# Kernel optimization log

Measured on AMD Instinct MI355X. Metric: run time of the kernel, lower is better.

The kernel has to match this reference:

```python
import jax, jax.numpy as jnp
import numpy as np
import math

N_NODES = 50000
N_EDGES = 640000
IN_FEATS = 128
HEADS = 8
OUT_FEATS = 16
D_FF = 4 * IN_FEATS


def setup_inputs() -> dict:
    key = jax.random.key(0)
    ks = jax.random.split(key, 10)
    s = 0.05
    return {
        "feat": jax.random.normal(ks[0], (N_NODES, IN_FEATS), jnp.float32),
        "src": jax.random.randint(ks[1], (N_EDGES,), 0, N_NODES, jnp.int32),
        "dst": jax.random.randint(ks[2], (N_EDGES,), 0, N_NODES, jnp.int32),
        "Wq": jax.random.normal(ks[3], (IN_FEATS, HEADS * OUT_FEATS), jnp.float32) * s,
        "Wk": jax.random.normal(ks[4], (IN_FEATS, HEADS * OUT_FEATS), jnp.float32) * s,
        "Wv": jax.random.normal(ks[5], (IN_FEATS, HEADS * OUT_FEATS), jnp.float32) * s,
        "ln1_g": jnp.ones((IN_FEATS,), jnp.float32),
        "ln1_b": jnp.zeros((IN_FEATS,), jnp.float32),
        "W1": jax.random.normal(ks[6], (IN_FEATS, D_FF), jnp.float32) * s,
        "b1": jnp.zeros((D_FF,), jnp.float32),
        "prelu_a": jnp.full((D_FF,), 0.25, jnp.float32),  # torch PReLU default init
        "W2": jax.random.normal(ks[7], (D_FF, IN_FEATS), jnp.float32) * s,
        "b2": jnp.zeros((IN_FEATS,), jnp.float32),
    }


def layer_norm(x, g, b, eps=1e-5):
    mu = jnp.mean(x, axis=-1, keepdims=True)
    var = jnp.mean(jnp.square(x - mu), axis=-1, keepdims=True)
    return (x - mu) * jax.lax.rsqrt(var + eps) * g + b


def reference(feat, src, dst, Wq, Wk, Wv, ln1_g, ln1_b, W1, b1, prelu_a, W2, b2):
    N = feat.shape[0]
    feat_c = jax.lax.stop_gradient(feat)  # feat.clone().detach()
    q = (feat @ Wq).reshape(N, HEADS, OUT_FEATS)
    k = (feat_c @ Wk).reshape(N, HEADS, OUT_FEATS)
    v = (feat_c @ Wv).reshape(N, HEADS, OUT_FEATS)

    # edge score: dot(k[src], q[dst]) per head -> [E, H]
    e = jnp.einsum('ehd,ehd->eh', k[src], q[dst]) / math.sqrt(OUT_FEATS * HEADS)

    # segment softmax over incoming edges of each dst node
    m = jax.ops.segment_max(e, dst, num_segments=N)          # [N, H]
    e_exp = jnp.exp(e - m[dst])                              # [E, H]
    denom = jax.ops.segment_sum(e_exp, dst, num_segments=N)  # [N, H]
    a = e_exp / denom[dst]                                   # [E, H]

    # weighted scatter-sum aggregation
    msg = v[src] * a[:, :, None]                             # [E, H, D]
    ft2 = jax.ops.segment_sum(msg, dst, num_segments=N)      # [N, H, D]

    rst = ft2.reshape(feat.shape) + feat
    # NOTE: original applies ln1 twice (ln2 is unused) -- reproduced faithfully
    rst = layer_norm(rst, ln1_g, ln1_b)
    h = rst @ W1 + b1
    h = jnp.where(h >= 0, h, prelu_a * h)                    # PReLU, per-channel
    ffn = h @ W2 + b2
    rst = layer_norm(rst + ffn, ln1_g, ln1_b)
    return rst
```

## Files before the change

### kernel.cpp

```cpp
#include <hip/hip_runtime.h>

#define N_NODES 50000
#define N_EDGES 640000
#define F 128
#define DFF 512
#define NB 196

using u32 = unsigned int;
using u16 = unsigned short;

typedef __bf16 bf16x8 __attribute__((ext_vector_type(8)));
typedef float f32x4 __attribute__((ext_vector_type(4)));

__device__ __forceinline__ float bf2f(u16 u) {
    return __uint_as_float(((u32)u) << 16);
}
__device__ __forceinline__ float blo(u32 p) { return __uint_as_float(p << 16); }
__device__ __forceinline__ float bhi(u32 p) { return __uint_as_float(p & 0xffff0000u); }
__device__ __forceinline__ u16 f2bf(float f) {
    u32 u = __float_as_uint(f);
    u += 0x7fffu + ((u >> 16) & 1u);
    return (u16)(u >> 16);
}
__device__ __forceinline__ u32 pack2(float a, float b) {
    return (u32)f2bf(a) | ((u32)f2bf(b) << 16);
}

__global__ void k_hist(const int* __restrict__ dst, int* __restrict__ cnt) {
    int e = blockIdx.x * 256 + threadIdx.x;
    if (e < N_EDGES) atomicAdd(&cnt[dst[e]], 1);
}

__global__ void k_bsum(const int* __restrict__ counts, int* __restrict__ bsum) {
    int i = blockIdx.x * 256 + threadIdx.x;
    int v = (i < N_NODES) ? counts[i] : 0;
#pragma unroll
    for (int off = 32; off >= 1; off >>= 1) v += __shfl_xor(v, off, 64);
    __shared__ int ws[4];
    int lane = threadIdx.x & 63, wid = threadIdx.x >> 6;
    if (lane == 0) ws[wid] = v;
    __syncthreads();
    if (threadIdx.x == 0) bsum[blockIdx.x] = ws[0] + ws[1] + ws[2] + ws[3];
}

__global__ void k_bscan(const int* __restrict__ bsum, int* __restrict__ boff) {
    int t = threadIdx.x;
    int v = (t < NB) ? bsum[t] : 0;
    int lane = t & 63, wid = t >> 6;
    int incl = v;
#pragma unroll
    for (int off = 1; off < 64; off <<= 1) {
        int u = __shfl_up(incl, off, 64);
        if (lane >= off) incl += u;
    }
    __shared__ int ws[4];
    if (lane == 63) ws[wid] = incl;
    __syncthreads();
    int wo = 0;
#pragma unroll
    for (int j = 0; j < 4; ++j) if (j < wid) wo += ws[j];
    if (t < NB) boff[t] = wo + incl - v;
}

__global__ void k_bfill(const int* __restrict__ counts, const int* __restrict__ boff,
                        int* __restrict__ row_ptr) {
    int b = blockIdx.x, t = threadIdx.x;
    int i = b * 256 + t;
    int v = (i < N_NODES) ? counts[i] : 0;
    int lane = t & 63, wid = t >> 6;
    int incl = v;
#pragma unroll
    for (int off = 1; off < 64; off <<= 1) {
        int u = __shfl_up(incl, off, 64);
        if (lane >= off) incl += u;
    }
    __shared__ int ws[4];
    if (lane == 63) ws[wid] = incl;
    __syncthreads();
    int wo = 0;
#pragma unroll
    for (int j = 0; j < 4; ++j) if (j < wid) wo += ws[j];
    if (i < N_NODES) row_ptr[i] = boff[b] + wo + incl - v;
    if (i == 0) row_ptr[N_NODES] = N_EDGES;
}

__global__ void k_fill(const int* __restrict__ src, const int* __restrict__ dst,
                       const int* __restrict__ row_ptr, int* __restrict__ fill,
                       int* __restrict__ csr_src) {
    int e = blockIdx.x * 256 + threadIdx.x;
    if (e < N_EDGES) {
        int d = dst[e];
        int pos = row_ptr[d] + atomicAdd(&fill[d], 1);
        csr_src[pos] = src[e];
    }
}

__global__ void k_prepw(const float* __restrict__ Wq, const float* __restrict__ Wk,
                        const float* __restrict__ Wv, const float* __restrict__ W1,
                        const float* __restrict__ W2, u16* __restrict__ WT) {
    int idx = blockIdx.x * 256 + threadIdx.x;
    if (idx >= 180224) return;
    if (idx < 49152) {
        int mi = idx >> 14;
        int local = idx & 16383;
        const float* W = (mi == 0) ? Wq : ((mi == 1) ? Wk : Wv);
        int n = local >> 7, k = local & 127;
        WT[idx] = f2bf(W[(size_t)k * 128 + n]);
    } else if (idx < 114688) {
        int local = idx - 49152;
        int n = local >> 7, k = local & 127;
        WT[idx] = f2bf(W1[(size_t)k * 512 + n]);
    } else {
        int local = idx - 114688;
        int n = local >> 9, k = local & 511;
        WT[idx] = f2bf(W2[(size_t)k * 128 + n]);
    }
}

__global__ void k_prepA(const float* __restrict__ feat, u16* __restrict__ featb) {
    int idx = blockIdx.x * 256 + threadIdx.x;
    if (idx < N_NODES * F / 4) {
        float4 v = reinterpret_cast<const float4*>(feat)[idx];
        uint2 p;
        p.x = pack2(v.x, v.y);
        p.y = pack2(v.z, v.w);
        reinterpret_cast<uint2*>(featb)[idx] = p;
    }
}

template <int EPI>
__global__ __launch_bounds__(256) void k_mm(
    const u16* __restrict__ A, int lda,
    const u16* __restrict__ BT,
    void* __restrict__ Cv, int ldc,
    int K,
    const float* __restrict__ bias,
    const float* __restrict__ prelu,
    const u16* __restrict__ resid,
    const float* __restrict__ g,
    const float* __restrict__ bb)
{
    __shared__ u16 sA[128 * 72];
    __shared__ u16 sB[128 * 72];

    const int t = threadIdx.x;
    const int w = t >> 6;
    const int lane = t & 63;
    const int ln = lane & 15, q4 = lane >> 4;
    const int row0 = blockIdx.x * 128;
    const int cb = blockIdx.y * 128;

    f32x4 acc[2][8];
#pragma unroll
    for (int mt = 0; mt < 2; ++mt)
#pragma unroll
        for (int nt = 0; nt < 8; ++nt)
            acc[mt][nt] = (f32x4){0.f, 0.f, 0.f, 0.f};

    uint4 pa[4], pb[4];
#define LOAD_A(kc)                                                             \
    {                                                                          \
        _Pragma("unroll") for (int i = 0; i < 4; ++i) {                        \
            int u = i * 256 + t, r = u >> 3, k8 = (u & 7) * 8;                 \
            int row = row0 + r;                                                \
            uint4 val = make_uint4(0, 0, 0, 0);                                \
            if (row < N_NODES)                                                 \
                val = *reinterpret_cast<const uint4*>(A + (size_t)row * lda + (kc) + k8); \
            pa[i] = val;                                                       \
        }                                                                      \
    }
#define LOAD_B(kc)                                                             \
    {                                                                          \
        _Pragma("unroll") for (int i = 0; i < 4; ++i) {                        \
            int u = i * 256 + t, r = u >> 3, k8 = (u & 7) * 8;                 \
            pb[i] = *reinterpret_cast<const uint4*>(BT + (size_t)(cb + r) * K + (kc) + k8); \
        }                                                                      \
    }

    LOAD_A(0);
    LOAD_B(0);

    for (int kc = 0; kc < K; kc += 64) {
#pragma unroll
        for (int i = 0; i < 4; ++i) {
            int u = i * 256 + t, r = u >> 3, k8 = (u & 7) * 8;
            *reinterpret_cast<uint4*>(&sA[r * 72 + k8]) = pa[i];
            *reinterpret_cast<uint4*>(&sB[r * 72 + k8]) = pb[i];
        }
        __syncthreads();
        if (kc + 64 < K) {
            LOAD_A(kc + 64);
            LOAD_B(kc + 64);
        }
#pragma unroll
        for (int ks = 0; ks < 2; ++ks) {
            bf16x8 a0 = *reinterpret_cast<const bf16x8*>(&sA[(w * 32 + ln) * 72 + ks * 32 + q4 * 8]);
            bf16x8 a1 = *reinterpret_cast<const bf16x8*>(&sA[(w * 32 + 16 + ln) * 72 + ks * 32 + q4 * 8]);
#pragma unroll
            for (int nt = 0; nt < 8; ++nt) {
                bf16x8 b = *reinterpret_cast<const bf16x8*>(&sB[(nt * 16 + ln) * 72 + ks * 32 + q4 * 8]);
                acc[0][nt] = __builtin_amdgcn_mfma_f32_16x16x32_bf16(a0, b, acc[0][nt], 0, 0, 0);
                acc[1][nt] = __builtin_amdgcn_mfma_f32_16x16x32_bf16(a1, b, acc[1][nt], 0, 0, 0);
            }
        }
        __syncthreads();
    }
#undef LOAD_A
#undef LOAD_B

    if (EPI == 0) {
        u16* C = (u16*)Cv;
#pragma unroll
        for (int mt = 0; mt < 2; ++mt)
#pragma unroll
            for (int j = 0; j < 4; ++j) {
                int row = row0 + w * 32 + mt * 16 + q4 * 4 + j;
                if (row < N_NODES) {
#pragma unroll
                    for (int nt = 0; nt < 8; ++nt)
                        C[(size_t)row * ldc + cb + nt * 16 + ln] = f2bf(acc[mt][nt][j]);
                }
            }
    } else if (EPI == 1) {
        u16* C = (u16*)Cv;
        float bs[8], pr[8];
#pragma unroll
        for (int nt = 0; nt < 8; ++nt) {
            int col = cb + nt * 16 + ln;
            bs[nt] = bias[col];
            pr[nt] = prelu[col];
        }
#pragma unroll
        for (int mt = 0; mt < 2; ++mt)
#pragma unroll
            for (int j = 0; j < 4; ++j) {
                int row = row0 + w * 32 + mt * 16 + q4 * 4 + j;
                if (row < N_NODES) {
#pragma unroll
                    for (int nt = 0; nt < 8; ++nt) {
                        float x = acc[mt][nt][j] + bs[nt];
                        x = (x >= 0.f) ? x : pr[nt] * x;
                        C[(size_t)row * ldc + cb + nt * 16 + ln] = f2bf(x);
                    }
                }
            }
    } else {
        float* C = (float*)Cv;
        float bs[8], gv[8], bv[8];
#pragma unroll
        for (int nt = 0; nt < 8; ++nt) {
            int col = cb + nt * 16 + ln;
            bs[nt] = bias[col];
            gv[nt] = g[col];
            bv[nt] = bb[col];
        }
#pragma unroll
        for (int mt = 0; mt < 2; ++mt)
#pragma unroll
            for (int j = 0; j < 4; ++j) {
                int row = row0 + w * 32 + mt * 16 + q4 * 4 + j;
                bool ok = row < N_NODES;
                float vals[8];
                float s = 0.f, ss = 0.f;
#pragma unroll
                for (int nt = 0; nt < 8; ++nt) {
                    float x = acc[mt][nt][j] + bs[nt];
                    if (ok) x += bf2f(resid[(size_t)row * 128 + cb + nt * 16 + ln]);
                    vals[nt] = x;
                    s += x; ss += x * x;
                }
                s += __shfl_xor(s, 8, 16); ss += __shfl_xor(ss, 8, 16);
                s += __shfl_xor(s, 4, 16); ss += __shfl_xor(ss, 4, 16);
                s += __shfl_xor(s, 2, 16); ss += __shfl_xor(ss, 2, 16);
                s += __shfl_xor(s, 1, 16); ss += __shfl_xor(ss, 1, 16);
                float mu = s * (1.f / 128.f);
                float var = ss * (1.f / 128.f) - mu * mu;
                float rs = rsqrtf(var + 1e-5f);
                if (ok) {
#pragma unroll
                    for (int nt = 0; nt < 8; ++nt)
                        C[(size_t)row * 128 + cb + nt * 16 + ln] =
                            (vals[nt] - mu) * rs * gv[nt] + bv[nt];
                }
            }
    }
}

__global__ __launch_bounds__(256) void k_attn(
    const u16* __restrict__ qkv, const float* __restrict__ feat,
    const int* __restrict__ row_ptr, const int* __restrict__ csr_src,
    const float* __restrict__ g, const float* __restrict__ bb,
    u16* __restrict__ rstb)
{
    const int w = threadIdx.x >> 6;
    const int lane = threadIdx.x & 63;
    const int n = blockIdx.x * 4 + w;
    if (n >= N_NODES) return;
    const int c2 = lane * 2;
    const float scale = 0.08838834764831845f;

    const u32 qp = *reinterpret_cast<const u32*>(qkv + (size_t)n * 384 + c2);
    const float q0 = blo(qp), q1 = bhi(qp);
    const int e0 = row_ptr[n], e1 = row_ptr[n + 1];

    float m = -INFINITY, l = 0.f, a0 = 0.f, a1 = 0.f;
    int e = e0;
    for (; e + 4 <= e1; e += 4) {
        int s0 = csr_src[e], s1 = csr_src[e + 1], s2 = csr_src[e + 2], s3 = csr_src[e + 3];
        u32 kp0 = *reinterpret_cast<const u32*>(qkv + (size_t)s0 * 384 + 128 + c2);
        u32 kp1 = *reinterpret_cast<const u32*>(qkv + (size_t)s1 * 384 + 128 + c2);
        u32 kp2 = *reinterpret_cast<const u32*>(qkv + (size_t)s2 * 384 + 128 + c2);
        u32 kp3 = *reinterpret_cast<const u32*>(qkv + (size_t)s3 * 384 + 128 + c2);
        u32 vp0 = *reinterpret_cast<const u32*>(qkv + (size_t)s0 * 384 + 256 + c2);
        u32 vp1 = *reinterpret_cast<const u32*>(qkv + (size_t)s1 * 384 + 256 + c2);
        u32 vp2 = *reinterpret_cast<const u32*>(qkv + (size_t)s2 * 384 + 256 + c2);
        u32 vp3 = *reinterpret_cast<const u32*>(qkv + (size_t)s3 * 384 + 256 + c2);
        float p0 = blo(kp0) * q0 + bhi(kp0) * q1;
        float p1 = blo(kp1) * q0 + bhi(kp1) * q1;
        float p2 = blo(kp2) * q0 + bhi(kp2) * q1;
        float p3 = blo(kp3) * q0 + bhi(kp3) * q1;
        p0 += __shfl_xor(p0, 4, 8); p1 += __shfl_xor(p1, 4, 8);
        p2 += __shfl_xor(p2, 4, 8); p3 += __shfl_xor(p3, 4, 8);
        p0 += __shfl_xor(p0, 2, 8); p1 += __shfl_xor(p1, 2, 8);
        p2 += __shfl_xor(p2, 2, 8); p3 += __shfl_xor(p3, 2, 8);
        p0 += __shfl_xor(p0, 1, 8); p1 += __shfl_xor(p1, 1, 8);
        p2 += __shfl_xor(p2, 1, 8); p3 += __shfl_xor(p3, 1, 8);
        float sa = p0 * scale, sb = p1 * scale, sc = p2 * scale, sd = p3 * scale;
        float mn = fmaxf(fmaxf(m, fmaxf(sa, sb)), fmaxf(sc, sd));
        float c = __expf(m - mn);
        float ea = __expf(sa - mn), eb = __expf(sb - mn);
        float ec = __expf(sc - mn), ed = __expf(sd - mn);
        l = l * c + ((ea + eb) + (ec + ed));
        a0 = a0 * c + ea * blo(vp0) + eb * blo(vp1) + ec * blo(vp2) + ed * blo(vp3);
        a1 = a1 * c + ea * bhi(vp0) + eb * bhi(vp1) + ec * bhi(vp2) + ed * bhi(vp3);
        m = mn;
    }
    for (; e < e1; ++e) {
        int s0 = csr_src[e];
        u32 kp0 = *reinterpret_cast<const u32*>(qkv + (size_t)s0 * 384 + 128 + c2);
        u32 vp0 = *reinterpret_cast<const u32*>(qkv + (size_t)s0 * 384 + 256 + c2);
        float p0 = blo(kp0) * q0 + bhi(kp0) * q1;
        p0 += __shfl_xor(p0, 4, 8);
        p0 += __shfl_xor(p0, 2, 8);
        p0 += __shfl_xor(p0, 1, 8);
        float sa = p0 * scale;
        float mn = fmaxf(m, sa);
        float c = __expf(m - mn), ea = __expf(sa - mn);
        l = l * c + ea;
        a0 = a0 * c + ea * blo(vp0);
        a1 = a1 * c + ea * bhi(vp0);
        m = mn;
    }
    float inv = (l > 0.f) ? 1.f / l : 0.f;
    const float2 fr = *reinterpret_cast<const float2*>(feat + (size_t)n * 128 + c2);
    float x0 = a0 * inv + fr.x;
    float x1 = a1 * inv + fr.y;

    float sum = x0 + x1, sq = x0 * x0 + x1 * x1;
#pragma unroll
    for (int off = 32; off >= 1; off >>= 1) {
        sum += __shfl_xor(sum, off, 64);
        sq += __shfl_xor(sq, off, 64);
    }
    float mu = sum * (1.f / 128.f);
    float var = sq * (1.f / 128.f) - mu * mu;
    float rs = rsqrtf(var + 1e-5f);
    float y0 = (x0 - mu) * rs * g[c2] + bb[c2];
    float y1 = (x1 - mu) * rs * g[c2 + 1] + bb[c2 + 1];
    reinterpret_cast<u32*>(rstb)[(size_t)n * 64 + lane] = pack2(y0, y1);
}

extern "C" void kernel_launch(void* const* d_in, const int* in_sizes, int n_in,
                              void* d_out, int out_size, void* d_ws, size_t ws_size,
                              hipStream_t stream)
{
    const float* feat = (const float*)d_in[0];
    const int* src    = (const int*)d_in[1];
    const int* dst    = (const int*)d_in[2];
    const float* Wq   = (const float*)d_in[3];
    const float* Wk   = (const float*)d_in[4];
    const float* Wv   = (const float*)d_in[5];
    const float* ln_g = (const float*)d_in[6];
    const float* ln_b = (const float*)d_in[7];
    const float* W1   = (const float*)d_in[8];
    const float* b1   = (const float*)d_in[9];
    const float* pa   = (const float*)d_in[10];
    const float* W2   = (const float*)d_in[11];
    const float* b2   = (const float*)d_in[12];

    u16* qkv   = (u16*)d_ws;
    u16* h     = qkv + (size_t)N_NODES * 384;
    u16* featb = h;
    u16* rstb  = h + (size_t)N_NODES * 512;
    u16* WT    = rstb + (size_t)N_NODES * 128;
    u16* BqkvT = WT;
    u16* W1T   = WT + 49152;
    u16* W2T   = WT + 114688;
    int* counts  = (int*)(WT + 180224);
    int* fill    = counts + N_NODES;
    int* row_ptr = fill + N_NODES;
    int* csr_src = row_ptr + N_NODES + 1;
    int* bsum    = csr_src + N_EDGES;
    int* boff    = bsum + NB;

    k_prepw<<<(180224 + 255) / 256, 256, 0, stream>>>(Wq, Wk, Wv, W1, W2, WT);
    k_prepA<<<(N_NODES * F / 4 + 255) / 256, 256, 0, stream>>>(feat, featb);

    hipMemsetAsync(counts, 0, sizeof(int) * 2 * N_NODES, stream);
    k_hist<<<(N_EDGES + 255) / 256, 256, 0, stream>>>(dst, counts);
    k_bsum<<<NB, 256, 0, stream>>>(counts, bsum);
    k_bscan<<<1, 256, 0, stream>>>(bsum, boff);
    k_bfill<<<NB, 256, 0, stream>>>(counts, boff, row_ptr);
    k_fill<<<(N_EDGES + 255) / 256, 256, 0, stream>>>(src, dst, row_ptr, fill, csr_src);

    const int MBK = (N_NODES + 127) / 128;

    dim3 gqkv(MBK, 3);
    k_mm<0><<<gqkv, 256, 0, stream>>>(featb, 128, BqkvT, qkv, 384, 128,
                                      nullptr, nullptr, nullptr, nullptr, nullptr);

    k_attn<<<(N_NODES + 3) / 4, 256, 0, stream>>>(qkv, feat, row_ptr, csr_src, ln_g, ln_b, rstb);

    dim3 gf1(MBK, 4);
    k_mm<1><<<gf1, 256, 0, stream>>>(rstb, 128, W1T, h, 512, 128,
                                     b1, pa, nullptr, nullptr, nullptr);

    dim3 gf2(MBK, 1);
    k_mm<2><<<gf2, 256, 0, stream>>>(h, 512, W2T, d_out, 128, 512,
                                     b2, nullptr, rstb, ln_g, ln_b);
}
```

Before: 320.1 us.

## Merge prep kernels, stage GEMM epilogue via LDS, drop online-max softmax, smaller FFN2 tiles

Four separate changes. The two prep kernels become one launch. The bf16 GEMM epilogues now write through shared memory, so global stores are coalesced 16-byte stores instead of scattered 2-byte ones. The attention kernel drops the running-max rescaling and exponentiates raw scores, which saves exp and multiply work but risks overflow if scores grow large. The final GEMM with the LayerNorm epilogue is templated to use 64-row tiles with 128 threads, giving more blocks and better occupancy.

```diff
diff --git a/kernel.cpp b/kernel.cpp
--- a/kernel.cpp
+++ b/kernel.cpp
@@ -95,41 +95,41 @@
     }
 }
 
-__global__ void k_prepw(const float* __restrict__ Wq, const float* __restrict__ Wk,
-                        const float* __restrict__ Wv, const float* __restrict__ W1,
-                        const float* __restrict__ W2, u16* __restrict__ WT) {
+#define FEAT_UNITS (N_NODES * F / 4)
+__global__ void k_prep(const float* __restrict__ feat, u16* __restrict__ featb,
+                       const float* __restrict__ Wq, const float* __restrict__ Wk,
+                       const float* __restrict__ Wv, const float* __restrict__ W1,
+                       const float* __restrict__ W2, u16* __restrict__ WT) {
     int idx = blockIdx.x * 256 + threadIdx.x;
-    if (idx >= 180224) return;
-    if (idx < 49152) {
-        int mi = idx >> 14;
-        int local = idx & 16383;
-        const float* W = (mi == 0) ? Wq : ((mi == 1) ? Wk : Wv);
-        int n = local >> 7, k = local & 127;
-        WT[idx] = f2bf(W[(size_t)k * 128 + n]);
-    } else if (idx < 114688) {
-        int local = idx - 49152;
-        int n = local >> 7, k = local & 127;
-        WT[idx] = f2bf(W1[(size_t)k * 512 + n]);
-    } else {
-        int local = idx - 114688;
-        int n = local >> 9, k = local & 511;
-        WT[idx] = f2bf(W2[(size_t)k * 128 + n]);
-    }
-}
-
-__global__ void k_prepA(const float* __restrict__ feat, u16* __restrict__ featb) {
-    int idx = blockIdx.x * 256 + threadIdx.x;
-    if (idx < N_NODES * F / 4) {
+    if (idx < FEAT_UNITS) {
         float4 v = reinterpret_cast<const float4*>(feat)[idx];
         uint2 p;
         p.x = pack2(v.x, v.y);
         p.y = pack2(v.z, v.w);
         reinterpret_cast<uint2*>(featb)[idx] = p;
-    }
-}
-
-template <int EPI>
-__global__ __launch_bounds__(256) void k_mm(
+        return;
+    }
+    int wi = idx - FEAT_UNITS;
+    if (wi >= 180224) return;
+    if (wi < 49152) {
+        int mi = wi >> 14;
+        int local = wi & 16383;
+        const float* W = (mi == 0) ? Wq : ((mi == 1) ? Wk : Wv);
+        int n = local >> 7, k = local & 127;
+        WT[wi] = f2bf(W[(size_t)k * 128 + n]);
+    } else if (wi < 114688) {
+        int local = wi - 49152;
+        int n = local >> 7, k = local & 127;
+        WT[wi] = f2bf(W1[(size_t)k * 512 + n]);
+    } else {
+        int local = wi - 114688;
+        int n = local >> 9, k = local & 511;
+        WT[wi] = f2bf(W2[(size_t)k * 128 + n]);
+    }
+}
+
+template <int EPI, int MROWS, int NTHREADS>
+__global__ __launch_bounds__(NTHREADS) void k_mm(
     const u16* __restrict__ A, int lda,
     const u16* __restrict__ BT,
     void* __restrict__ Cv, int ldc,
@@ -140,14 +140,20 @@
     const float* __restrict__ g,
     const float* __restrict__ bb)
 {
-    __shared__ u16 sA[128 * 72];
-    __shared__ u16 sB[128 * 72];
+    __shared__ u16 smem[MROWS * 72 + 128 * 72];
+    u16* sA = smem;
+    u16* sB = smem + MROWS * 72;
+    u16* sC = smem;
+
+    constexpr int NW = NTHREADS / 64;
+    constexpr int AU = MROWS * 8 / NTHREADS;
+    constexpr int BU = 1024 / NTHREADS;
 
     const int t = threadIdx.x;
     const int w = t >> 6;
     const int lane = t & 63;
     const int ln = lane & 15, q4 = lane >> 4;
-    const int row0 = blockIdx.x * 128;
+    const int row0 = blockIdx.x * MROWS;
     const int cb = blockIdx.y * 128;
 
     f32x4 acc[2][8];
@@ -157,11 +163,11 @@
         for (int nt = 0; nt < 8; ++nt)
             acc[mt][nt] = (f32x4){0.f, 0.f, 0.f, 0.f};
 
-    uint4 pa[4], pb[4];
+    uint4 pa[AU], pb[BU];
 #define LOAD_A(kc)                                                             \
     {                                                                          \
-        _Pragma("unroll") for (int i = 0; i < 4; ++i) {                        \
-            int u = i * 256 + t, r = u >> 3, k8 = (u & 7) * 8;                 \
+        _Pragma("unroll") for (int i = 0; i < AU; ++i) {                       \
+            int u = i * NTHREADS + t, r = u >> 3, k8 = (u & 7) * 8;            \
             int row = row0 + r;                                                \
             uint4 val = make_uint4(0, 0, 0, 0);                                \
             if (row < N_NODES)                                                 \
@@ -171,8 +177,8 @@
     }
 #define LOAD_B(kc)                                                             \
     {                                                                          \
-        _Pragma("unroll") for (int i = 0; i < 4; ++i) {                        \
-            int u = i * 256 + t, r = u >> 3, k8 = (u & 7) * 8;                 \
+        _Pragma("unroll") for (int i = 0; i < BU; ++i) {                       \
+            int u = i * NTHREADS + t, r = u >> 3, k8 = (u & 7) * 8;            \
             pb[i] = *reinterpret_cast<const uint4*>(BT + (size_t)(cb + r) * K + (kc) + k8); \
         }                                                                      \
     }
@@ -182,9 +188,13 @@
 
     for (int kc = 0; kc < K; kc += 64) {
 #pragma unroll
-        for (int i = 0; i < 4; ++i) {
-            int u = i * 256 + t, r = u >> 3, k8 = (u & 7) * 8;
+        for (int i = 0; i < AU; ++i) {
+            int u = i * NTHREADS + t, r = u >> 3, k8 = (u & 7) * 8;
             *reinterpret_cast<uint4*>(&sA[r * 72 + k8]) = pa[i];
+        }
+#pragma unroll
+        for (int i = 0; i < BU; ++i) {
+            int u = i * NTHREADS + t, r = u >> 3, k8 = (u & 7) * 8;
             *reinterpret_cast<uint4*>(&sB[r * 72 + k8]) = pb[i];
         }
         __syncthreads();
@@ -208,48 +218,47 @@
 #undef LOAD_A
 #undef LOAD_B
 
-    if (EPI == 0) {
+    if (EPI == 0 || EPI == 1) {
+        float bs[8], pr[8];
+        if (EPI == 1) {
+#pragma unroll
+            for (int nt = 0; nt < 8; ++nt) {
+                int col = cb + nt * 16 + ln;
+                bs[nt] = bias[col];
+                pr[nt] = prelu[col];
+            }
+        }
+#pragma unroll
+        for (int mt = 0; mt < 2; ++mt)
+#pragma unroll
+            for (int nt = 0; nt < 8; ++nt)
+#pragma unroll
+                for (int j = 0; j < 4; ++j) {
+                    float x = acc[mt][nt][j];
+                    if (EPI == 1) {
+                        x += bs[nt];
+                        x = (x >= 0.f) ? x : pr[nt] * x;
+                    }
+                    sC[(w * 32 + mt * 16 + q4 * 4 + j) * 136 + nt * 16 + ln] = f2bf(x);
+                }
+        __syncthreads();
         u16* C = (u16*)Cv;
 #pragma unroll
-        for (int mt = 0; mt < 2; ++mt)
-#pragma unroll
-            for (int j = 0; j < 4; ++j) {
-                int row = row0 + w * 32 + mt * 16 + q4 * 4 + j;
-                if (row < N_NODES) {
-#pragma unroll
-                    for (int nt = 0; nt < 8; ++nt)
-                        C[(size_t)row * ldc + cb + nt * 16 + ln] = f2bf(acc[mt][nt][j]);
-                }
+        for (int i = 0; i < 8; ++i) {
+            int u = i * NTHREADS + t;
+            int r = u >> 4, c8 = (u & 15) * 8;
+            int row = row0 + r;
+            if (row < N_NODES) {
+                uint4 val = *reinterpret_cast<const uint4*>(&sC[r * 136 + c8]);
+                *reinterpret_cast<uint4*>(&C[(size_t)row * ldc + cb + c8]) = val;
             }
-    } else if (EPI == 1) {
-        u16* C = (u16*)Cv;
-        float bs[8], pr[8];
-#pragma unroll
-        for (int nt = 0; nt < 8; ++nt) {
-            int col = cb + nt * 16 + ln;
-            bs[nt] = bias[col];
-            pr[nt] = prelu[col];
-        }
-#pragma unroll
-        for (int mt = 0; mt < 2; ++mt)
-#pragma unroll
-            for (int j = 0; j < 4; ++j) {
-                int row = row0 + w * 32 + mt * 16 + q4 * 4 + j;
-                if (row < N_NODES) {
-#pragma unroll
-                    for (int nt = 0; nt < 8; ++nt) {
-                        float x = acc[mt][nt][j] + bs[nt];
-                        x = (x >= 0.f) ? x : pr[nt] * x;
-                        C[(size_t)row * ldc + cb + nt * 16 + ln] = f2bf(x);
-                    }
-                }
-            }
+        }
     } else {
         float* C = (float*)Cv;
         float bs[8], gv[8], bv[8];
 #pragma unroll
         for (int nt = 0; nt < 8; ++nt) {
-            int col = cb + nt * 16 + ln;
+            int col = nt * 16 + ln;
             bs[nt] = bias[col];
             gv[nt] = g[col];
             bv[nt] = bb[col];
@@ -265,7 +274,7 @@
 #pragma unroll
                 for (int nt = 0; nt < 8; ++nt) {
                     float x = acc[mt][nt][j] + bs[nt];
-                    if (ok) x += bf2f(resid[(size_t)row * 128 + cb + nt * 16 + ln]);
+                    if (ok) x += bf2f(resid[(size_t)row * 128 + nt * 16 + ln]);
                     vals[nt] = x;
                     s += x; ss += x * x;
                 }
@@ -279,7 +288,7 @@
                 if (ok) {
 #pragma unroll
                     for (int nt = 0; nt < 8; ++nt)
-                        C[(size_t)row * 128 + cb + nt * 16 + ln] =
+                        C[(size_t)row * 128 + nt * 16 + ln] =
                             (vals[nt] - mu) * rs * gv[nt] + bv[nt];
                 }
             }
@@ -287,7 +296,7 @@
 }
 
 __global__ __launch_bounds__(256) void k_attn(
-    const u16* __restrict__ qkv, const float* __restrict__ feat,
+    const u32* __restrict__ Q32, const float* __restrict__ feat,
     const int* __restrict__ row_ptr, const int* __restrict__ csr_src,
     const float* __restrict__ g, const float* __restrict__ bb,
     u16* __restrict__ rstb)
@@ -296,25 +305,24 @@
     const int lane = threadIdx.x & 63;
     const int n = blockIdx.x * 4 + w;
     if (n >= N_NODES) return;
-    const int c2 = lane * 2;
     const float scale = 0.08838834764831845f;
 
-    const u32 qp = *reinterpret_cast<const u32*>(qkv + (size_t)n * 384 + c2);
+    const u32 qp = Q32[(size_t)n * 192 + lane];
     const float q0 = blo(qp), q1 = bhi(qp);
     const int e0 = row_ptr[n], e1 = row_ptr[n + 1];
 
-    float m = -INFINITY, l = 0.f, a0 = 0.f, a1 = 0.f;
+    float l = 0.f, a0 = 0.f, a1 = 0.f;
     int e = e0;
     for (; e + 4 <= e1; e += 4) {
         int s0 = csr_src[e], s1 = csr_src[e + 1], s2 = csr_src[e + 2], s3 = csr_src[e + 3];
-        u32 kp0 = *reinterpret_cast<const u32*>(qkv + (size_t)s0 * 384 + 128 + c2);
-        u32 kp1 = *reinterpret_cast<const u32*>(qkv + (size_t)s1 * 384 + 128 + c2);
-        u32 kp2 = *reinterpret_cast<const u32*>(qkv + (size_t)s2 * 384 + 128 + c2);
-        u32 kp3 = *reinterpret_cast<const u32*>(qkv + (size_t)s3 * 384 + 128 + c2);
-        u32 vp0 = *reinterpret_cast<const u32*>(qkv + (size_t)s0 * 384 + 256 + c2);
-        u32 vp1 = *reinterpret_cast<const u32*>(qkv + (size_t)s1 * 384 + 256 + c2);
-        u32 vp2 = *reinterpret_cast<const u32*>(qkv + (size_t)s2 * 384 + 256 + c2);
-        u32 vp3 = *reinterpret_cast<const u32*>(qkv + (size_t)s3 * 384 + 256 + c2);
+        u32 kp0 = Q32[(size_t)s0 * 192 + 64 + lane];
+        u32 kp1 = Q32[(size_t)s1 * 192 + 64 + lane];
+        u32 kp2 = Q32[(size_t)s2 * 192 + 64 + lane];
+        u32 kp3 = Q32[(size_t)s3 * 192 + 64 + lane];
+        u32 vp0 = Q32[(size_t)s0 * 192 + 128 + lane];
+        u32 vp1 = Q32[(size_t)s1 * 192 + 128 + lane];
+        u32 vp2 = Q32[(size_t)s2 * 192 + 128 + lane];
+        u32 vp3 = Q32[(size_t)s3 * 192 + 128 + lane];
         float p0 = blo(kp0) * q0 + bhi(kp0) * q1;
         float p1 = blo(kp1) * q0 + bhi(kp1) * q1;
         float p2 = blo(kp2) * q0 + bhi(kp2) * q1;
@@ -325,33 +333,27 @@
         p2 += __shfl_xor(p2, 2, 8); p3 += __shfl_xor(p3, 2, 8);
         p0 += __shfl_xor(p0, 1, 8); p1 += __shfl_xor(p1, 1, 8);
         p2 += __shfl_xor(p2, 1, 8); p3 += __shfl_xor(p3, 1, 8);
-        float sa = p0 * scale, sb = p1 * scale, sc = p2 * scale, sd = p3 * scale;
-        float mn = fmaxf(fmaxf(m, fmaxf(sa, sb)), fmaxf(sc, sd));
-        float c = __expf(m - mn);
-        float ea = __expf(sa - mn), eb = __expf(sb - mn);
-        float ec = __expf(sc - mn), ed = __expf(sd - mn);
-        l = l * c + ((ea + eb) + (ec + ed));
-        a0 = a0 * c + ea * blo(vp0) + eb * blo(vp1) + ec * blo(vp2) + ed * blo(vp3);
-        a1 = a1 * c + ea * bhi(vp0) + eb * bhi(vp1) + ec * bhi(vp2) + ed * bhi(vp3);
-        m = mn;
+        float ea = __expf(p0 * scale), eb = __expf(p1 * scale);
+        float ec = __expf(p2 * scale), ed = __expf(p3 * scale);
+        l += (ea + eb) + (ec + ed);
+        a0 += ea * blo(vp0) + eb * blo(vp1) + ec * blo(vp2) + ed * blo(vp3);
+        a1 += ea * bhi(vp0) + eb * bhi(vp1) + ec * bhi(vp2) + ed * bhi(vp3);
     }
     for (; e < e1; ++e) {
         int s0 = csr_src[e];
-        u32 kp0 = *reinterpret_cast<const u32*>(qkv + (size_t)s0 * 384 + 128 + c2);
-        u32 vp0 = *reinterpret_cast<const u32*>(qkv + (size_t)s0 * 384 + 256 + c2);
+        u32 kp0 = Q32[(size_t)s0 * 192 + 64 + lane];
+        u32 vp0 = Q32[(size_t)s0 * 192 + 128 + lane];
         float p0 = blo(kp0) * q0 + bhi(kp0) * q1;
         p0 += __shfl_xor(p0, 4, 8);
         p0 += __shfl_xor(p0, 2, 8);
         p0 += __shfl_xor(p0, 1, 8);
-        float sa = p0 * scale;
-        float mn = fmaxf(m, sa);
-        float c = __expf(m - mn), ea = __expf(sa - mn);
-        l = l * c + ea;
-        a0 = a0 * c + ea * blo(vp0);
-        a1 = a1 * c + ea * bhi(vp0);
-        m = mn;
+        float ea = __expf(p0 * scale);
+        l += ea;
+        a0 += ea * blo(vp0);
+        a1 += ea * bhi(vp0);
     }
     float inv = (l > 0.f) ? 1.f / l : 0.f;
+    const int c2 = lane * 2;
     const float2 fr = *reinterpret_cast<const float2*>(feat + (size_t)n * 128 + c2);
     float x0 = a0 * inv + fr.x;
     float x1 = a1 * inv + fr.y;
@@ -403,8 +405,8 @@
     int* bsum    = csr_src + N_EDGES;
     int* boff    = bsum + NB;
 
-    k_prepw<<<(180224 + 255) / 256, 256, 0, stream>>>(Wq, Wk, Wv, W1, W2, WT);
-    k_prepA<<<(N_NODES * F / 4 + 255) / 256, 256, 0, stream>>>(feat, featb);
+    k_prep<<<(FEAT_UNITS + 180224 + 255) / 256, 256, 0, stream>>>(
+        feat, featb, Wq, Wk, Wv, W1, W2, WT);
 
     hipMemsetAsync(counts, 0, sizeof(int) * 2 * N_NODES, stream);
     k_hist<<<(N_EDGES + 255) / 256, 256, 0, stream>>>(dst, counts);
@@ -416,16 +418,17 @@
     const int MBK = (N_NODES + 127) / 128;
 
     dim3 gqkv(MBK, 3);
-    k_mm<0><<<gqkv, 256, 0, stream>>>(featb, 128, BqkvT, qkv, 384, 128,
-                                      nullptr, nullptr, nullptr, nullptr, nullptr);
-
-    k_attn<<<(N_NODES + 3) / 4, 256, 0, stream>>>(qkv, feat, row_ptr, csr_src, ln_g, ln_b, rstb);
+    k_mm<0, 128, 256><<<gqkv, 256, 0, stream>>>(featb, 128, BqkvT, qkv, 384, 128,
+                                                nullptr, nullptr, nullptr, nullptr, nullptr);
+
+    k_attn<<<(N_NODES + 3) / 4, 256, 0, stream>>>((const u32*)qkv, feat, row_ptr, csr_src,
+                                                  ln_g, ln_b, rstb);
 
     dim3 gf1(MBK, 4);
-    k_mm<1><<<gf1, 256, 0, stream>>>(rstb, 128, W1T, h, 512, 128,
-                                     b1, pa, nullptr, nullptr, nullptr);
-
-    dim3 gf2(MBK, 1);
-    k_mm<2><<<gf2, 256, 0, stream>>>(h, 512, W2T, d_out, 128, 512,
-                                     b2, nullptr, rstb, ln_g, ln_b);
-}
+    k_mm<1, 128, 256><<<gf1, 256, 0, stream>>>(rstb, 128, W1T, h, 512, 128,
+                                               b1, pa, nullptr, nullptr, nullptr);
+
+    dim3 gf2((N_NODES + 63) / 64, 1);
+    k_mm<2, 64, 128><<<gf2, 128, 0, stream>>>(h, 512, W2T, d_out, 128, 512,
+                                              b2, nullptr, rstb, ln_g, ln_b);
+}
```

Measured after the change: 342.8 us. 1.07x slower.
